# Kernel tuning notes

Hardware: AMD Instinct MI355X
Metric: run time of the kernel (lower is better)

## Reference

```python
import jax, jax.numpy as jnp
import numpy as np

H = 16        # query heads
HK = 8        # kv heads
D = 128       # head dim
HID = 2048    # hidden size
FF = 6144     # mlp intermediate
THETA = 1e6   # rope base (qwen3)
EPS = 1e-6
T = 2048      # total tokens


def rmsnorm(x, w):
    return x * jax.lax.rsqrt(jnp.mean(x * x, axis=-1, keepdims=True) + EPS) * w


def rope(pos, x):
    # x: [T, h, D], rotate-half RoPE
    half = D // 2
    inv = 1.0 / (THETA ** (jnp.arange(half, dtype=jnp.float32) / half))
    freqs = pos.astype(jnp.float32)[:, None] * inv          # [T, half]
    cos = jnp.cos(freqs)[:, None, :]
    sin = jnp.sin(freqs)[:, None, :]
    x1, x2 = x[..., :half], x[..., half:]
    return jnp.concatenate([x1 * cos - x2 * sin, x2 * cos + x1 * sin], axis=-1)


def setup_inputs() -> dict:
    key = jax.random.key(0)
    ks = jax.random.split(key, 12)
    s = 0.02
    return {
        "positions": jnp.arange(T, dtype=jnp.int32),
        "hidden_states": jax.random.normal(ks[0], (T, HID), dtype=jnp.float32),
        "wq": jax.random.normal(ks[1], (H * D, HID), dtype=jnp.float32) * s,
        "wk": jax.random.normal(ks[2], (HK * D, HID), dtype=jnp.float32) * s,
        "wv": jax.random.normal(ks[3], (HK * D, HID), dtype=jnp.float32) * s,
        "wo": jax.random.normal(ks[4], (HID, H * D), dtype=jnp.float32) * s,
        "q_norm_w": jnp.ones((D,), dtype=jnp.float32),
        "k_norm_w": jnp.ones((D,), dtype=jnp.float32),
        "ln1_w": jnp.ones((HID,), dtype=jnp.float32),
        "ln2_w": jnp.ones((HID,), dtype=jnp.float32),
        "w_gate": jax.random.normal(ks[5], (FF, HID), dtype=jnp.float32) * s,
        "w_up": jax.random.normal(ks[6], (FF, HID), dtype=jnp.float32) * s,
        "w_down": jax.random.normal(ks[7], (HID, FF), dtype=jnp.float32) * s,
    }


def reference(positions, hidden_states, wq, wk, wv, wo, q_norm_w, k_norm_w,
              ln1_w, ln2_w, w_gate, w_up, w_down):
    t = hidden_states.shape[0]
    residual = hidden_states
    h = rmsnorm(hidden_states, ln1_w)
    q = (h @ wq.T).reshape(t, H, D)
    k = (h @ wk.T).reshape(t, HK, D)
    v = (h @ wv.T).reshape(t, HK, D)
    q = rmsnorm(q, q_norm_w)
    k = rmsnorm(k, k_norm_w)
    q = rope(positions, q)
    k = rope(positions, k)
    # GQA: expand kv heads to query heads
    g = H // HK
    kr = jnp.repeat(k, g, axis=1)  # [t, H, D]
    vr = jnp.repeat(v, g, axis=1)
    scores = jnp.einsum('thd,shd->hts', q, kr) * (D ** -0.5)
    causal = positions[:, None] >= positions[None, :]
    scores = jnp.where(causal[None], scores, jnp.finfo(scores.dtype).min)
    p = jax.nn.softmax(scores, axis=-1)
    o = jnp.einsum('hts,shd->thd', p, vr).reshape(t, H * D)
    h = residual + o @ wo.T
    residual = h
    h = rmsnorm(h, ln2_w)
    h = (jax.nn.silu(h @ w_gate.T) * (h @ w_up.T)) @ w_down.T
    return residual + h
```

## Files before the change

### kernel.cpp

```cpp
#include <hip/hip_runtime.h>
#include <hip/hip_bf16.h>
#include <stdint.h>

namespace {

constexpr int kT   = 2048;
constexpr int kHid = 2048;
constexpr int kH   = 16;
constexpr int kHK  = 8;
constexpr int kD   = 128;
constexpr int kFF  = 6144;

using bf16x8 = __attribute__((ext_vector_type(8))) short;
using f32x4  = __attribute__((ext_vector_type(4))) float;

__device__ __forceinline__ float bf2f(unsigned short u) {
    return __uint_as_float(((unsigned)u) << 16);
}
__device__ __forceinline__ unsigned short f2bf(float f) {
    unsigned u = __float_as_uint(f);
    return (unsigned short)((u + 0x7fffu + ((u >> 16) & 1u)) >> 16);
}
__device__ __forceinline__ void gload_lds16(const void* g, void* l) {
    __builtin_amdgcn_global_load_lds(
        (__attribute__((address_space(1))) void*)g,
        (__attribute__((address_space(3))) void*)l, 16, 0, 0);
}
__device__ __forceinline__ f32x4 mf(bf16x8 a, bf16x8 b, f32x4 c) {
    return __builtin_amdgcn_mfma_f32_16x16x32_bf16(a, b, c, 0, 0, 0);
}

__global__ __launch_bounds__(256)
void cvt_f32_bf16(const float* __restrict__ src, unsigned short* __restrict__ dst, int n4) {
    int i = blockIdx.x * 256 + threadIdx.x;
    if (i < n4) {
        float4 v = ((const float4*)src)[i];
        ushort4 o;
        o.x = f2bf(v.x); o.y = f2bf(v.y); o.z = f2bf(v.z); o.w = f2bf(v.w);
        ((ushort4*)dst)[i] = o;
    }
}

__global__ __launch_bounds__(256)
void reduce2(const float* __restrict__ p0, const float* __restrict__ p1,
             const float* __restrict__ res, float* __restrict__ out, int n4) {
    int i = blockIdx.x * 256 + threadIdx.x;
    if (i < n4) {
        float4 a = ((const float4*)p0)[i];
        float4 b = ((const float4*)p1)[i];
        float4 r = ((const float4*)res)[i];
        float4 o;
        o.x = a.x + b.x + r.x;
        o.y = a.y + b.y + r.y;
        o.z = a.z + b.z + r.z;
        o.w = a.w + b.w + r.w;
        ((float4*)out)[i] = o;
    }
}

__global__ __launch_bounds__(256)
void rmsnorm_k(const float* __restrict__ x, const float* __restrict__ w,
               unsigned short* __restrict__ out) {
    const int row = blockIdx.x;
    const int tid = threadIdx.x;
    const float4* xr = (const float4*)(x + (size_t)row * kHid);
    float4 v0 = xr[tid];
    float4 v1 = xr[tid + 256];
    float ss = v0.x*v0.x + v0.y*v0.y + v0.z*v0.z + v0.w*v0.w
             + v1.x*v1.x + v1.y*v1.y + v1.z*v1.z + v1.w*v1.w;
#pragma unroll
    for (int m = 1; m < 64; m <<= 1) ss += __shfl_xor(ss, m);
    __shared__ float red[4];
    if ((tid & 63) == 0) red[tid >> 6] = ss;
    __syncthreads();
    float tot = red[0] + red[1] + red[2] + red[3];
    float rs = rsqrtf(tot * (1.0f / kHid) + 1e-6f);
    const float4* wv = (const float4*)w;
    float4 w0 = wv[tid], w1 = wv[tid + 256];
    ushort4 o0, o1;
    o0.x = f2bf(v0.x * rs * w0.x); o0.y = f2bf(v0.y * rs * w0.y);
    o0.z = f2bf(v0.z * rs * w0.z); o0.w = f2bf(v0.w * rs * w0.w);
    o1.x = f2bf(v1.x * rs * w1.x); o1.y = f2bf(v1.y * rs * w1.y);
    o1.z = f2bf(v1.z * rs * w1.z); o1.w = f2bf(v1.w * rs * w1.w);
    ushort4* orow = (ushort4*)(out + (size_t)row * kHid);
    orow[tid] = o0;
    orow[tid + 256] = o1;
}

template <int EPI>
__global__ __launch_bounds__(512, 2)
void gemm128(const unsigned short* __restrict__ A,
             const unsigned short* __restrict__ B,
             void* __restrict__ C,
             int M, int N, int K, int KS,
             float* __restrict__ p0, float* __restrict__ p1) {
    __shared__ unsigned short smem[2][3][128 * 64];

    const int tid  = threadIdx.x;
    const int lane = tid & 63;
    const int l15  = lane & 15;
    const int g4   = lane >> 4;
    const int wid  = tid >> 6;
    const int wr   = wid >> 2;
    const int wc   = wid & 3;
    const int bm   = blockIdx.y * 128;
    const int bn   = blockIdx.x * 256;
    const int kb   = (EPI == 4) ? blockIdx.z * KS : 0;
    const int NT   = ((EPI == 4) ? KS : K) >> 6;
    const int NI   = NT >> 1;

    f32x4 acc[4][4] = {};

    auto stage = [&](int b, int reg, int t) {
        const unsigned short* Base = (reg == 0) ? A : B;
        const int br = (reg == 0) ? bm : bn + (reg - 1) * 128;
#pragma unroll
        for (int i = 0; i < 2; ++i) {
            int ch   = tid + i * 512;
            int row  = ch >> 3;
            int slot = (ch & 7) ^ (row & 7);
            gload_lds16(Base + (size_t)(br + row) * K + kb + t * 64 + slot * 8,
                        (char*)&smem[b][reg][0] + ch * 16);
        }
    };
    auto rdA = [&](int b, int m, int ks) {
        int row = wr * 64 + m * 16 + l15;
        return *(const bf16x8*)((const char*)&smem[b][0][0]
               + row * 128 + (((ks * 4 + g4) ^ (row & 7)) * 16));
    };
    auto rdB = [&](int b, int n, int ks) {
        int row = wc * 64 + n * 16 + l15;
        return *(const bf16x8*)((const char*)&smem[b][1 + (row >> 7)][0]
               + (row & 127) * 128 + (((ks * 4 + g4) ^ (row & 7)) * 16));
    };

    stage(0, 1, 0); stage(0, 2, 0); stage(0, 0, 0);
    stage(1, 1, 1); stage(1, 2, 1);
    asm volatile("s_waitcnt vmcnt(4)" ::: "memory");
    __builtin_amdgcn_s_barrier();

    for (int i = 0; i < NI; ++i) {
        const int e  = 2 * i;
        const int o  = e + 1;
        const bool pf = (e + 2 < NT);
        bf16x8 af[4][2], bfr[4][2];

#pragma unroll
        for (int m = 0; m < 4; ++m) { af[m][0] = rdA(0, m, 0); af[m][1] = rdA(0, m, 1); }
#pragma unroll
        for (int n = 0; n < 4; ++n) { bfr[n][0] = rdB(0, n, 0); bfr[n][1] = rdB(0, n, 1); }
        stage(1, 0, o);
        __builtin_amdgcn_s_barrier();
        asm volatile("s_waitcnt lgkmcnt(0)" ::: "memory");
        __builtin_amdgcn_sched_barrier(0);
        __builtin_amdgcn_s_setprio(1);
#pragma unroll
        for (int m = 0; m < 4; ++m) {
            acc[m][0] = mf(af[m][0], bfr[0][0], acc[m][0]);
            acc[m][0] = mf(af[m][1], bfr[0][1], acc[m][0]);
        }
        __builtin_amdgcn_s_setprio(0);
        __builtin_amdgcn_s_barrier();

        if (pf) stage(0, 1, e + 2);
        __builtin_amdgcn_s_barrier();
        __builtin_amdgcn_s_setprio(1);
#pragma unroll
        for (int m = 0; m < 4; ++m) {
            acc[m][1] = mf(af[m][0], bfr[1][0], acc[m][1]);
            acc[m][1] = mf(af[m][1], bfr[1][1], acc[m][1]);
        }
        __builtin_amdgcn_s_setprio(0);
        __builtin_amdgcn_s_barrier();

        if (pf) stage(0, 2, e + 2);
        __builtin_amdgcn_s_barrier();
        __builtin_amdgcn_s_setprio(1);
#pragma unroll
        for (int m = 0; m < 4; ++m) {
            acc[m][2] = mf(af[m][0], bfr[2][0], acc[m][2]);
            acc[m][2] = mf(af[m][1], bfr[2][1], acc[m][2]);
        }
        __builtin_amdgcn_s_setprio(0);
        __builtin_amdgcn_s_barrier();

        __builtin_amdgcn_s_setprio(1);
#pragma unroll
        for (int m = 0; m < 4; ++m) {
            acc[m][3] = mf(af[m][0], bfr[3][0], acc[m][3]);
            acc[m][3] = mf(af[m][1], bfr[3][1], acc[m][3]);
        }
        __builtin_amdgcn_s_setprio(0);
        if (pf) asm volatile("s_waitcnt vmcnt(4)" ::: "memory");
        else    asm volatile("s_waitcnt vmcnt(0)" ::: "memory");
        __builtin_amdgcn_s_barrier();

#pragma unroll
        for (int m = 0; m < 4; ++m) { af[m][0] = rdA(1, m, 0); af[m][1] = rdA(1, m, 1); }
#pragma unroll
        for (int n = 0; n < 4; ++n) { bfr[n][0] = rdB(1, n, 0); bfr[n][1] = rdB(1, n, 1); }
        if (pf) stage(0, 0, e + 2);
        __builtin_amdgcn_s_barrier();
        asm volatile("s_waitcnt lgkmcnt(0)" ::: "memory");
        __builtin_amdgcn_sched_barrier(0);
        __builtin_amdgcn_s_setprio(1);
#pragma unroll
        for (int m = 0; m < 4; ++m) {
            acc[m][0] = mf(af[m][0], bfr[0][0], acc[m][0]);
            acc[m][0] = mf(af[m][1], bfr[0][1], acc[m][0]);
        }
        __builtin_amdgcn_s_setprio(0);
        __builtin_amdgcn_s_barrier();

        if (pf) stage(1, 1, o + 2);
        __builtin_amdgcn_s_barrier();
        __builtin_amdgcn_s_setprio(1);
#pragma unroll
        for (int m = 0; m < 4; ++m) {
            acc[m][1] = mf(af[m][0], bfr[1][0], acc[m][1]);
            acc[m][1] = mf(af[m][1], bfr[1][1], acc[m][1]);
        }
        __builtin_amdgcn_s_setprio(0);
        __builtin_amdgcn_s_barrier();

        if (pf) stage(1, 2, o + 2);
        __builtin_amdgcn_s_barrier();
        __builtin_amdgcn_s_setprio(1);
#pragma unroll
        for (int m = 0; m < 4; ++m) {
            acc[m][2] = mf(af[m][0], bfr[2][0], acc[m][2]);
            acc[m][2] = mf(af[m][1], bfr[2][1], acc[m][2]);
        }
        __builtin_amdgcn_s_setprio(0);
        __builtin_amdgcn_s_barrier();

        __builtin_amdgcn_s_setprio(1);
#pragma unroll
        for (int m = 0; m < 4; ++m) {
            acc[m][3] = mf(af[m][0], bfr[3][0], acc[m][3]);
            acc[m][3] = mf(af[m][1], bfr[3][1], acc[m][3]);
        }
        __builtin_amdgcn_s_setprio(0);
        if (pf) asm volatile("s_waitcnt vmcnt(4)" ::: "memory");
        __builtin_amdgcn_s_barrier();
    }

    float* P = nullptr;
    if (EPI == 4) P = (blockIdx.z == 0) ? p0 : p1;
#pragma unroll
    for (int m = 0; m < 4; ++m) {
#pragma unroll
        for (int n = 0; n < 4; ++n) {
            int row = bm + wr * 64 + m * 16 + g4 * 4;
            int col = bn + wc * 64 + n * 16 + l15;
#pragma unroll
            for (int r = 0; r < 4; ++r) {
                size_t idx = (size_t)(row + r) * N + col;
                float v = acc[m][n][r];
                if (EPI == 0) ((float*)C)[idx] = v;
                else          P[idx] = v;
            }
        }
    }
}

__global__ __launch_bounds__(512, 2)
void gemm_gu(const unsigned short* __restrict__ A,
             const unsigned short* __restrict__ WGp,
             const unsigned short* __restrict__ WUp,
             unsigned short* __restrict__ OUT) {
    __shared__ unsigned short smem[2][4][128 * 64];

    const int tid  = threadIdx.x;
    const int lane = tid & 63;
    const int l15  = lane & 15;
    const int g4   = lane >> 4;
    const int wid  = tid >> 6;
    const int wr   = wid >> 1;
    const int wc   = wid & 1;
    const int bm   = blockIdx.y * 256;
    const int bn2  = blockIdx.x * 128;
    const int K    = kHid;
    const int NT   = K >> 6;
    const int NI   = NT >> 1;

    f32x4 accg[4][4] = {};
    f32x4 accu[4][4] = {};

    auto stage = [&](int b, int reg, int t) {
        const unsigned short* Base = (reg == 2) ? WGp : (reg == 3) ? WUp : A;
        const int br = (reg < 2) ? (bm + reg * 128) : bn2;
#pragma unroll
        for (int i = 0; i < 2; ++i) {
            int ch   = tid + i * 512;
            int row  = ch >> 3;
            int slot = (ch & 7) ^ (row & 7);
            gload_lds16(Base + (size_t)(br + row) * K + t * 64 + slot * 8,
                        (char*)&smem[b][reg][0] + ch * 16);
        }
    };
    auto rdA = [&](int b, int m, int ks) {
        int rt  = wr * 64 + m * 16 + l15;
        int row = rt & 127;
        return *(const bf16x8*)((const char*)&smem[b][rt >> 7][0]
               + row * 128 + (((ks * 4 + g4) ^ (row & 7)) * 16));
    };
    auto rdB = [&](int b, int reg, int n, int ks) {
        int row = wc * 64 + n * 16 + l15;
        return *(const bf16x8*)((const char*)&smem[b][reg][0]
               + row * 128 + (((ks * 4 + g4) ^ (row & 7)) * 16));
    };

    stage(0, 2, 0); stage(0, 3, 0); stage(0, 0, 0); stage(0, 1, 0);
    stage(1, 2, 1); stage(1, 0, 1); stage(1, 1, 1);
    asm volatile("s_waitcnt vmcnt(6)" ::: "memory");
    __builtin_amdgcn_s_barrier();

    for (int i = 0; i < NI; ++i) {
        const int e  = 2 * i;
        const int o  = e + 1;
        const bool pf = (e + 2 < NT);
        bf16x8 af[4][2], bg[4][2], bu[4][2];

#pragma unroll
        for (int m = 0; m < 4; ++m) { af[m][0] = rdA(0, m, 0); af[m][1] = rdA(0, m, 1); }
#pragma unroll
        for (int n = 0; n < 4; ++n) { bg[n][0] = rdB(0, 2, n, 0); bg[n][1] = rdB(0, 2, n, 1); }
        stage(1, 3, o);
        __builtin_amdgcn_s_barrier();
        asm volatile("s_waitcnt lgkmcnt(0)" ::: "memory");
        __builtin_amdgcn_sched_barrier(0);
        __builtin_amdgcn_s_setprio(1);
#pragma unroll
        for (int m = 0; m < 4; ++m)
#pragma unroll
            for (int n = 0; n < 2; ++n) {
                accg[m][n] = mf(af[m][0], bg[n][0], accg[m][n]);
                accg[m][n] = mf(af[m][1], bg[n][1], accg[m][n]);
            }
        __builtin_amdgcn_s_setprio(0);
        __builtin_amdgcn_s_barrier();

        if (pf) stage(0, 2, e + 2);
        __builtin_amdgcn_s_barrier();
        __builtin_amdgcn_s_setprio(1);
#pragma unroll
        for (int m = 0; m < 4; ++m)
#pragma unroll
            for (int n = 2; n < 4; ++n) {
                accg[m][n] = mf(af[m][0], bg[n][0], accg[m][n]);
                accg[m][n] = mf(af[m][1], bg[n][1], accg[m][n]);
            }
        __builtin_amdgcn_s_setprio(0);
        __builtin_amdgcn_s_barrier();

#pragma unroll
        for (int n = 0; n < 4; ++n) { bu[n][0] = rdB(0, 3, n, 0); bu[n][1] = rdB(0, 3, n, 1); }
        if (pf) stage(0, 0, e + 2);
        __builtin_amdgcn_s_barrier();
        asm volatile("s_waitcnt lgkmcnt(0)" ::: "memory");
        __builtin_amdgcn_sched_barrier(0);
        __builtin_amdgcn_s_setprio(1);
#pragma unroll
        for (int m = 0; m < 4; ++m)
#pragma unroll
            for (int n = 0; n < 2; ++n) {
                accu[m][n] = mf(af[m][0], bu[n][0], accu[m][n]);
                accu[m][n] = mf(af[m][1], bu[n][1], accu[m][n]);
            }
        __builtin_amdgcn_s_setprio(0);
        __builtin_amdgcn_s_barrier();

        if (pf) stage(0, 1, e + 2);
        __builtin_amdgcn_s_barrier();
        __builtin_amdgcn_s_setprio(1);
#pragma unroll
        for (int m = 0; m < 4; ++m)
#pragma unroll
            for (int n = 2; n < 4; ++n) {
                accu[m][n] = mf(af[m][0], bu[n][0], accu[m][n]);
                accu[m][n] = mf(af[m][1], bu[n][1], accu[m][n]);
            }
        __builtin_amdgcn_s_setprio(0);
        if (pf) asm volatile("s_waitcnt vmcnt(6)" ::: "memory");
        else    asm volatile("s_waitcnt vmcnt(0)" ::: "memory");
        __builtin_amdgcn_s_barrier();

#pragma unroll
        for (int m = 0; m < 4; ++m) { af[m][0] = rdA(1, m, 0); af[m][1] = rdA(1, m, 1); }
#pragma unroll
        for (int n = 0; n < 4; ++n) { bg[n][0] = rdB(1, 2, n, 0); bg[n][1] = rdB(1, 2, n, 1); }
        if (pf) stage(0, 3, e + 2);
        __builtin_amdgcn_s_barrier();
        asm volatile("s_waitcnt lgkmcnt(0)" ::: "memory");
        __builtin_amdgcn_sched_barrier(0);
        __builtin_amdgcn_s_setprio(1);
#pragma unroll
        for (int m = 0; m < 4; ++m)
#pragma unroll
            for (int n = 0; n < 2; ++n) {
                accg[m][n] = mf(af[m][0], bg[n][0], accg[m][n]);
                accg[m][n] = mf(af[m][1], bg[n][1], accg[m][n]);
            }
        __builtin_amdgcn_s_setprio(0);
        __builtin_amdgcn_s_barrier();

        if (pf) stage(1, 2, o + 2);
        __builtin_amdgcn_s_barrier();
        __builtin_amdgcn_s_setprio(1);
#pragma unroll
        for (int m = 0; m < 4; ++m)
#pragma unroll
            for (int n = 2; n < 4; ++n) {
                accg[m][n] = mf(af[m][0], bg[n][0], accg[m][n]);
                accg[m][n] = mf(af[m][1], bg[n][1], accg[m][n]);
            }
        __builtin_amdgcn_s_setprio(0);
        __builtin_amdgcn_s_barrier();

#pragma unroll
        for (int n = 0; n < 4; ++n) { bu[n][0] = rdB(1, 3, n, 0); bu[n][1] = rdB(1, 3, n, 1); }
        if (pf) stage(1, 0, o + 2);
        __builtin_amdgcn_s_barrier();
        asm volatile("s_waitcnt lgkmcnt(0)" ::: "memory");
        __builtin_amdgcn_sched_barrier(0);
        __builtin_amdgcn_s_setprio(1);
#pragma unroll
        for (int m = 0; m < 4; ++m)
#pragma unroll
            for (int n = 0; n < 2; ++n) {
                accu[m][n] = mf(af[m][0], bu[n][0], accu[m][n]);
                accu[m][n] = mf(af[m][1], bu[n][1], accu[m][n]);
            }
        __builtin_amdgcn_s_setprio(0);
        __builtin_amdgcn_s_barrier();

        if (pf) stage(1, 1, o + 2);
        __builtin_amdgcn_s_barrier();
        __builtin_amdgcn_s_setprio(1);
#pragma unroll
        for (int m = 0; m < 4; ++m)
#pragma unroll
            for (int n = 2; n < 4; ++n) {
                accu[m][n] = mf(af[m][0], bu[n][0], accu[m][n]);
                accu[m][n] = mf(af[m][1], bu[n][1], accu[m][n]);
            }
        __builtin_amdgcn_s_setprio(0);
        if (pf) asm volatile("s_waitcnt vmcnt(6)" ::: "memory");
        __builtin_amdgcn_s_barrier();
    }

#pragma unroll
    for (int m = 0; m < 4; ++m) {
#pragma unroll
        for (int n = 0; n < 4; ++n) {
            int row = bm + wr * 64 + m * 16 + g4 * 4;
            int col = bn2 + wc * 64 + n * 16 + l15;
#pragma unroll
            for (int r = 0; r < 4; ++r) {
                float g = accg[m][n][r];
                float u = accu[m][n][r];
                OUT[(size_t)(row + r) * kFF + col] = f2bf(g / (1.0f + __expf(-g)) * u);
            }
        }
    }
}

__global__ __launch_bounds__(256)
void qknorm_rope(const float* __restrict__ qkv, const int* __restrict__ positions,
                 const float* __restrict__ qnw, const float* __restrict__ knw,
                 unsigned short* __restrict__ Qo, unsigned short* __restrict__ Ko) {
    const int t    = blockIdx.x;
    const int j    = blockIdx.y * 4 + (threadIdx.x >> 6);
    const int lane = threadIdx.x & 63;
    const float* src = qkv + (size_t)t * 4096 + j * 128;
    float x1 = src[lane];
    float x2 = src[lane + 64];
    float ss = x1 * x1 + x2 * x2;
#pragma unroll
    for (int m = 1; m < 64; m <<= 1) ss += __shfl_xor(ss, m);
    float rs = rsqrtf(ss * (1.0f / 128.0f) + 1e-6f);
    const float* w = (j < 16) ? qnw : knw;
    float n1 = x1 * rs * w[lane];
    float n2 = x2 * rs * w[lane + 64];
    float inv = powf(1.0e6f, -(float)lane * (1.0f / 64.0f));
    float fr = (float)positions[t] * inv;
    float sn, cs;
    sincosf(fr, &sn, &cs);
    float o1 = n1 * cs - n2 * sn;
    float o2 = n2 * cs + n1 * sn;
    if (j < 16) {
        unsigned short* d = Qo + (size_t)t * (kH * kD) + j * kD;
        d[lane] = f2bf(o1);
        d[lane + 64] = f2bf(o2);
    } else {
        unsigned short* d = Ko + (size_t)t * (kHK * kD) + (j - 16) * kD;
        d[lane] = f2bf(o1);
        d[lane + 64] = f2bf(o2);
    }
}

__global__ __launch_bounds__(256)
void vtrans(const float* __restrict__ qkv, unsigned short* __restrict__ Vt) {
    __shared__ float tile[32][33];
    const int t0 = blockIdx.x * 32;
    const int d0 = blockIdx.y * 32;
    const int tc = threadIdx.x & 31;
    const int tr = threadIdx.x >> 5;
#pragma unroll
    for (int i = 0; i < 4; ++i) {
        int trow = tr + i * 8;
        tile[trow][tc] = qkv[(size_t)(t0 + trow) * 4096 + 3072 + d0 + tc];
    }
    __syncthreads();
#pragma unroll
    for (int i = 0; i < 4; ++i) {
        int drow = tr + i * 8;
        Vt[(size_t)(d0 + drow) * kT + t0 + tc] = f2bf(tile[tc][drow]);
    }
}

__global__ __launch_bounds__(512, 4)
void attn_fwd5(const unsigned short* __restrict__ Q,
               const unsigned short* __restrict__ Kc,
               const unsigned short* __restrict__ Vt,
               unsigned short* __restrict__ O) {
    __shared__ unsigned short Kb[2][64 * 128];
    __shared__ unsigned short Vb[2][128 * 64];
    __shared__ float MergeML[4][2][64];

    const int tid  = threadIdx.x;
    const int lane = tid & 63;
    const int l15  = lane & 15;
    const int g4   = lane >> 4;
    const int wid  = tid >> 6;
    const int s    = wid & 1;
    const int grp  = wid >> 1;
    const int hs   = grp >> 1;
    const int qsub = grp & 1;
    const int hkk  = blockIdx.x;
    const int h    = hkk * 2 + hs;
    const int nby  = gridDim.y;
    const int by   = blockIdx.y;
    const int byl  = (by & 1) ? (nby - 1 - (by >> 1)) : (by >> 1);
    const int q0   = byl * 32 + qsub * 16;
    const int nch  = byl / 2 + 1;
    const int c0   = (nch + 1) >> 1;
    const int myn  = s ? (nch - c0) : c0;
    const int qi   = q0 + l15;
    const int vt   = grp * 64 + lane;

    const int addrA = ((g4 & 1) * 32 + l15) * 4;
    const int addrB = addrA + 64;
    const int addrQ = g4 * 80;
    const bool hb   = (g4 >> 1) != 0;

    bf16x8 qf[4];
#pragma unroll
    for (int ks = 0; ks < 4; ++ks)
        qf[ks] = *(const bf16x8*)(Q + (size_t)(q0 + l15) * (kH * kD) + h * kD + ks * 32 + g4 * 8);

    f32x4 oacc[8] = {};
    float mrun = -3e38f, lrun = 0.f;
    const float scale = 0.08838834764831845f;

    auto stage = [&](int kv0) {
#pragma unroll
        for (int i = 0; i < 4; ++i) {
            int ch  = vt + i * 256;
            int row = ch >> 4;
            int c16 = ch & 15;
            gload_lds16(Kc + (size_t)(kv0 + row) * (kHK * kD) + hkk * kD
                            + ((c16 ^ (row & 7)) * 8),
                        (char*)Kb[s] + ch * 16);
        }
#pragma unroll
        for (int i = 0; i < 4; ++i) {
            int ch  = vt + i * 256;
            int row = ch >> 3;
            int c8  = ch & 7;
            gload_lds16(Vt + (size_t)(hkk * kD + row) * kT + kv0
                            + ((c8 ^ (row & 7)) * 8),
                        (char*)Vb[s] + ch * 16);
        }
    };

    for (int c = 0; c < c0; ++c) {
        const bool act = c < myn;
        const int kv0 = (s ? (c0 + c) : c) * 64;
        if (act) stage(kv0);
        asm volatile("s_waitcnt vmcnt(0)" ::: "memory");
        __builtin_amdgcn_s_barrier();
        __builtin_amdgcn_sched_barrier(0);

        if (act) {
            f32x4 sa[4] = {};
            __builtin_amdgcn_s_setprio(1);
#pragma unroll
            for (int hh = 0; hh < 4; ++hh) {
                const int row = hh * 16 + l15;
#pragma unroll
                for (int ks = 0; ks < 4; ++ks) {
                    bf16x8 kf = *(const bf16x8*)((const char*)Kb[s]
                                  + row * 256 + (((ks * 4 + g4) ^ (row & 7)) * 16));
                    sa[hh] = mf(kf, qf[ks], sa[hh]);
                }
            }
            __builtin_amdgcn_s_setprio(0);

            float sv[4][4];
#pragma unroll
            for (int hh = 0; hh < 4; ++hh)
#pragma unroll
                for (int r = 0; r < 4; ++r)
                    sv[hh][r] = sa[hh][r] * scale;
            if (kv0 + 63 > q0) {
#pragma unroll
                for (int hh = 0; hh < 4; ++hh)
#pragma unroll
                    for (int r = 0; r < 4; ++r) {
                        int ki = kv0 + hh * 16 + g4 * 4 + r;
                        if (ki > qi) sv[hh][r] = -3e38f;
                    }
            }

            float m16;
            {
                float a = fmaxf(fmaxf(sv[0][0], sv[0][1]), fmaxf(sv[0][2], sv[0][3]));
                float b2 = fmaxf(fmaxf(sv[1][0], sv[1][1]), fmaxf(sv[1][2], sv[1][3]));
                float c2 = fmaxf(fmaxf(sv[2][0], sv[2][1]), fmaxf(sv[2][2], sv[2][3]));
                float d2 = fmaxf(fmaxf(sv[3][0], sv[3][1]), fmaxf(sv[3][2], sv[3][3]));
                m16 = fmaxf(fmaxf(a, b2), fmaxf(c2, d2));
            }
            m16 = fmaxf(m16, __shfl_xor(m16, 16));
            m16 = fmaxf(m16, __shfl_xor(m16, 32));

            if (__any(m16 > mrun)) {
                float mnew = fmaxf(mrun, m16);
                float corr = __expf(mrun - mnew);
                mrun = mnew;
                lrun *= corr;
                float cr[4];
#pragma unroll
                for (int r = 0; r < 4; ++r)
                    cr[r] = __int_as_float(__builtin_amdgcn_ds_bpermute(
                                addrQ + 4 * r, __float_as_int(corr)));
#pragma unroll
                for (int c2 = 0; c2 < 8; ++c2)
#pragma unroll
                    for (int r = 0; r < 4; ++r)
                        oacc[c2][r] *= cr[r];
            }

            float p[4][4];
            float ps = 0.f;
#pragma unroll
            for (int hh = 0; hh < 4; ++hh)
#pragma unroll
                for (int r = 0; r < 4; ++r) {
                    float pe = __expf(sv[hh][r] - mrun);
                    p[hh][r] = pe;
                    ps += pe;
                }
            ps += __shfl_xor(ps, 16);
            ps += __shfl_xor(ps, 32);
            lrun += ps;

            unsigned pk[4][2];
#pragma unroll
            for (int hh = 0; hh < 4; ++hh) {
                asm("v_cvt_pk_bf16_f32 %0, %1, %2"
                    : "=v"(pk[hh][0]) : "v"(p[hh][0]), "v"(p[hh][1]));
                asm("v_cvt_pk_bf16_f32 %0, %1, %2"
                    : "=v"(pk[hh][1]) : "v"(p[hh][2]), "v"(p[hh][3]));
            }
            int ex[4][2][2];
#pragma unroll
            for (int hh = 0; hh < 4; ++hh)
#pragma unroll
                for (int ii = 0; ii < 2; ++ii) {
                    ex[hh][ii][0] = __builtin_amdgcn_ds_bpermute(addrA, (int)pk[hh][ii]);
                    ex[hh][ii][1] = __builtin_amdgcn_ds_bpermute(addrB, (int)pk[hh][ii]);
                }
            union { int w[4]; bf16x8 v; } pu0, pu1;
#pragma unroll
            for (int jw = 0; jw < 4; ++jw) {
                pu0.w[jw] = hb ? ex[1][jw & 1][jw >> 1] : ex[0][jw & 1][jw >> 1];
                pu1.w[jw] = hb ? ex[3][jw & 1][jw >> 1] : ex[2][jw & 1][jw >> 1];
            }
            bf16x8 pa0 = pu0.v;
            bf16x8 pa1 = pu1.v;

            __builtin_amdgcn_s_setprio(1);
#pragma unroll
            for (int c2 = 0; c2 < 8; ++c2) {
                const int d = c2 * 16 + l15;
                bf16x8 vf0 = *(const bf16x8*)((const char*)Vb[s]
                              + d * 128 + ((g4 ^ (d & 7)) * 16));
                oacc[c2] = mf(pa0, vf0, oacc[c2]);
                bf16x8 vf1 = *(const bf16x8*)((const char*)Vb[s]
                              + d * 128 + ((((4 + g4) ^ (d & 7))) * 16));
                oacc[c2] = mf(pa1, vf1, oacc[c2]);
            }
            __builtin_amdgcn_s_setprio(0);
        }
        __builtin_amdgcn_s_barrier();
    }

    float* KbF = (float*)&Kb[0][0];
    if (s == 1) {
        MergeML[grp][0][lane] = mrun;
        MergeML[grp][1][lane] = lrun;
#pragma unroll
        for (int c2 = 0; c2 < 8; ++c2)
#pragma unroll
            for (int r = 0; r < 4; ++r)
                KbF[grp * 2048 + (c2 * 4 + r) * 64 + lane] = oacc[c2][r];
    }
    asm volatile("s_waitcnt lgkmcnt(0)" ::: "memory");
    __builtin_amdgcn_s_barrier();

    if (s == 0) {
        float m1 = MergeML[grp][0][lane];
        float l1 = MergeML[grp][1][lane];
        float mg = fmaxf(mrun, m1);
        float a0 = __expf(mrun - mg);
        float a1 = __expf(m1 - mg);
        float L  = lrun * a0 + l1 * a1;
        float ar0[4], ar1[4], Lr[4];
#pragma unroll
        for (int r = 0; r < 4; ++r) {
            ar0[r] = __int_as_float(__builtin_amdgcn_ds_bpermute(
                         addrQ + 4 * r, __float_as_int(a0)));
            ar1[r] = __int_as_float(__builtin_amdgcn_ds_bpermute(
                         addrQ + 4 * r, __float_as_int(a1)));
            Lr[r]  = __int_as_float(__builtin_amdgcn_ds_bpermute(
                         addrQ + 4 * r, __float_as_int(L)));
        }
#pragma unroll
        for (int c2 = 0; c2 < 8; ++c2)
#pragma unroll
            for (int r = 0; r < 4; ++r) {
                float oex = KbF[grp * 2048 + (c2 * 4 + r) * 64 + lane];
                float v = (oacc[c2][r] * ar0[r] + oex * ar1[r]) / Lr[r];
                O[(size_t)(q0 + g4 * 4 + r) * (kH * kD) + h * kD + c2 * 16 + l15] = f2bf(v);
            }
    }
}

}

extern "C" void kernel_launch(void* const* d_in, const int* in_sizes, int n_in,
                              void* d_out, int out_size, void* d_ws, size_t ws_size,
                              hipStream_t stream) {
    (void)in_sizes; (void)n_in; (void)out_size; (void)ws_size;

    const int*   positions = (const int*)  d_in[0];
    const float* hidden    = (const float*)d_in[1];
    const float* wq  = (const float*)d_in[2];
    const float* wk  = (const float*)d_in[3];
    const float* wv  = (const float*)d_in[4];
    const float* wo  = (const float*)d_in[5];
    const float* qnw = (const float*)d_in[6];
    const float* knw = (const float*)d_in[7];
    const float* ln1 = (const float*)d_in[8];
    const float* ln2 = (const float*)d_in[9];
    const float* wg  = (const float*)d_in[10];
    const float* wu  = (const float*)d_in[11];
    const float* wd  = (const float*)d_in[12];

    char* ws = (char*)d_ws;
    unsigned short* WQKV = (unsigned short*)(ws + 0);
    unsigned short* WO   = (unsigned short*)(ws + 16777216);
    unsigned short* WG   = (unsigned short*)(ws + 25165824);
    unsigned short* WU   = (unsigned short*)(ws + 50331648);
    unsigned short* WD   = (unsigned short*)(ws + 75497472);
    unsigned short* XN1  = (unsigned short*)(ws + 100663296);
    unsigned short* OATT = (unsigned short*)(ws + 109051904);
    float*          H1   = (float*)(ws + 117440512);
    unsigned short* XN2  = (unsigned short*)(ws + 134217728);
    float*          QKVF = (float*)(ws + 142606336);
    unsigned short* QB   = (unsigned short*)(ws + 176160768);
    unsigned short* KB   = (unsigned short*)(ws + 184549376);
    unsigned short* VT   = (unsigned short*)(ws + 188743680);
    unsigned short* ACT  = (unsigned short*)(ws + 167772160);

    float* OP0 = (float*)(ws + 142606336);
    float* OP1 = (float*)(ws + 159383552);
    float* DP0 = (float*)(ws + 0);
    float* DP1 = (float*)(ws + 16777216);

    auto cvt = [&](const float* s, unsigned short* dst, size_t n) {
        int n4 = (int)(n / 4);
        cvt_f32_bf16<<<dim3((n4 + 255) / 256), dim3(256), 0, stream>>>(s, dst, n4);
    };

    cvt(wq, WQKV,                 (size_t)kH  * kD * kHid);
    cvt(wk, WQKV + 2048 * kHid,   (size_t)kHK * kD * kHid);
    cvt(wv, WQKV + 3072 * kHid,   (size_t)kHK * kD * kHid);
    cvt(wo, WO,                   (size_t)kHid * kH * kD);
    cvt(wg, WG,                   (size_t)kFF * kHid);
    cvt(wu, WU,                   (size_t)kFF * kHid);
    cvt(wd, WD,                   (size_t)kHid * kFF);

    rmsnorm_k<<<dim3(kT), dim3(256), 0, stream>>>(hidden, ln1, XN1);

    gemm128<0><<<dim3(4096 / 256, kT / 128), dim3(512), 0, stream>>>(
        XN1, WQKV, QKVF, kT, 4096, kHid, kHid, nullptr, nullptr);

    qknorm_rope<<<dim3(kT, 6), dim3(256), 0, stream>>>(QKVF, positions, qnw, knw, QB, KB);
    vtrans<<<dim3(kT / 32, 1024 / 32), dim3(256), 0, stream>>>(QKVF, VT);

    attn_fwd5<<<dim3(kHK, kT / 32), dim3(512), 0, stream>>>(QB, KB, VT, OATT);

    gemm128<4><<<dim3(kHid / 256, kT / 128, 2), dim3(512), 0, stream>>>(
        OATT, WO, nullptr, kT, kHid, kHid, 1024, OP0, OP1);
    reduce2<<<dim3(kT * kHid / 4 / 256), dim3(256), 0, stream>>>(
        OP0, OP1, hidden, H1, kT * kHid / 4);

    rmsnorm_k<<<dim3(kT), dim3(256), 0, stream>>>(H1, ln2, XN2);

    gemm_gu<<<dim3(kFF / 128, kT / 256), dim3(512), 0, stream>>>(XN2, WG, WU, ACT);

    gemm128<4><<<dim3(kHid / 256, kT / 128, 2), dim3(512), 0, stream>>>(
        ACT, WD, nullptr, kT, kHid, kFF, 3072, DP0, DP1);
    reduce2<<<dim3(kT * kHid / 4 / 256), dim3(256), 0, stream>>>(
        DP0, DP1, H1, (float*)d_out, kT * kHid / 4);
}
```

Measured before the change: 396.6 us.

## Use 256x256 split-K-4 GEMMs, fuse reduction into RMSNorm, retile gate/up GEMM

```diff
diff --git a/kernel.cpp b/kernel.cpp
--- a/kernel.cpp
+++ b/kernel.cpp
@@ -42,18 +42,21 @@
 }
 
 __global__ __launch_bounds__(256)
-void reduce2(const float* __restrict__ p0, const float* __restrict__ p1,
+void reduce4(const float* __restrict__ p0, const float* __restrict__ p1,
+             const float* __restrict__ p2, const float* __restrict__ p3,
              const float* __restrict__ res, float* __restrict__ out, int n4) {
     int i = blockIdx.x * 256 + threadIdx.x;
     if (i < n4) {
         float4 a = ((const float4*)p0)[i];
         float4 b = ((const float4*)p1)[i];
+        float4 c = ((const float4*)p2)[i];
+        float4 d = ((const float4*)p3)[i];
         float4 r = ((const float4*)res)[i];
         float4 o;
-        o.x = a.x + b.x + r.x;
-        o.y = a.y + b.y + r.y;
-        o.z = a.z + b.z + r.z;
-        o.w = a.w + b.w + r.w;
+        o.x = a.x + b.x + c.x + d.x + r.x;
+        o.y = a.y + b.y + c.y + d.y + r.y;
+        o.z = a.z + b.z + c.z + d.z + r.z;
+        o.w = a.w + b.w + c.w + d.w + r.w;
         ((float4*)out)[i] = o;
     }
 }
@@ -87,6 +90,265 @@
     orow[tid + 256] = o1;
 }
 
+__global__ __launch_bounds__(256)
+void rmsnorm_red4(const float* __restrict__ p0, const float* __restrict__ p1,
+                  const float* __restrict__ p2, const float* __restrict__ p3,
+                  const float* __restrict__ res, const float* __restrict__ w,
+                  float* __restrict__ H, unsigned short* __restrict__ out) {
+    const int row = blockIdx.x;
+    const int tid = threadIdx.x;
+    const size_t base = (size_t)row * kHid;
+    float4 v0, v1;
+    {
+        const float4* a = (const float4*)(p0 + base);
+        const float4* b = (const float4*)(p1 + base);
+        const float4* c = (const float4*)(p2 + base);
+        const float4* d = (const float4*)(p3 + base);
+        const float4* r = (const float4*)(res + base);
+        float4 a0 = a[tid], b0 = b[tid], c0 = c[tid], d0 = d[tid], r0 = r[tid];
+        v0.x = a0.x + b0.x + c0.x + d0.x + r0.x;
+        v0.y = a0.y + b0.y + c0.y + d0.y + r0.y;
+        v0.z = a0.z + b0.z + c0.z + d0.z + r0.z;
+        v0.w = a0.w + b0.w + c0.w + d0.w + r0.w;
+        float4 a1 = a[tid + 256], b1 = b[tid + 256], c1 = c[tid + 256],
+               d1 = d[tid + 256], r1 = r[tid + 256];
+        v1.x = a1.x + b1.x + c1.x + d1.x + r1.x;
+        v1.y = a1.y + b1.y + c1.y + d1.y + r1.y;
+        v1.z = a1.z + b1.z + c1.z + d1.z + r1.z;
+        v1.w = a1.w + b1.w + c1.w + d1.w + r1.w;
+    }
+    ((float4*)(H + base))[tid] = v0;
+    ((float4*)(H + base))[tid + 256] = v1;
+    float ss = v0.x*v0.x + v0.y*v0.y + v0.z*v0.z + v0.w*v0.w
+             + v1.x*v1.x + v1.y*v1.y + v1.z*v1.z + v1.w*v1.w;
+#pragma unroll
+    for (int m = 1; m < 64; m <<= 1) ss += __shfl_xor(ss, m);
+    __shared__ float red[4];
+    if ((tid & 63) == 0) red[tid >> 6] = ss;
+    __syncthreads();
+    float tot = red[0] + red[1] + red[2] + red[3];
+    float rs = rsqrtf(tot * (1.0f / kHid) + 1e-6f);
+    const float4* wv = (const float4*)w;
+    float4 w0 = wv[tid], w1 = wv[tid + 256];
+    ushort4 o0, o1;
+    o0.x = f2bf(v0.x * rs * w0.x); o0.y = f2bf(v0.y * rs * w0.y);
+    o0.z = f2bf(v0.z * rs * w0.z); o0.w = f2bf(v0.w * rs * w0.w);
+    o1.x = f2bf(v1.x * rs * w1.x); o1.y = f2bf(v1.y * rs * w1.y);
+    o1.z = f2bf(v1.z * rs * w1.z); o1.w = f2bf(v1.w * rs * w1.w);
+    ushort4* orow = (ushort4*)(out + base);
+    orow[tid] = o0;
+    orow[tid + 256] = o1;
+}
+
+template <int EPI>
+__global__ __launch_bounds__(512, 2)
+void gemm256(const unsigned short* __restrict__ A,
+             const unsigned short* __restrict__ B,
+             void* __restrict__ C,
+             int M, int N, int K, int KS,
+             float* __restrict__ p0, float* __restrict__ p1,
+             float* __restrict__ p2, float* __restrict__ p3) {
+    __shared__ unsigned short smem[2][4][128 * 64];
+
+    const int tid  = threadIdx.x;
+    const int lane = tid & 63;
+    const int l15  = lane & 15;
+    const int g4   = lane >> 4;
+    const int wid  = tid >> 6;
+    const int wr   = wid >> 2;
+    const int wc   = wid & 3;
+    const int bm   = blockIdx.y * 256;
+    const int bn   = blockIdx.x * 256;
+    const int kb   = (EPI == 4) ? blockIdx.z * KS : 0;
+    const int NT   = ((EPI == 4) ? KS : K) >> 6;
+    const int NI   = NT >> 1;
+
+    f32x4 acc[8][4] = {};
+
+    auto stage = [&](int b, int reg, int t) {
+        const unsigned short* Base = (reg < 2) ? A : B;
+        const int br = ((reg < 2) ? bm : bn) + (reg & 1) * 128;
+#pragma unroll
+        for (int i = 0; i < 2; ++i) {
+            int ch   = tid + i * 512;
+            int row  = ch >> 3;
+            int slot = (ch & 7) ^ (row & 7);
+            gload_lds16(Base + (size_t)(br + row) * K + kb + t * 64 + slot * 8,
+                        (char*)&smem[b][reg][0] + ch * 16);
+        }
+    };
+    auto rdA = [&](int b, int m, int ks) {
+        int row = m * 16 + l15;
+        return *(const bf16x8*)((const char*)&smem[b][wr][0]
+               + row * 128 + (((ks * 4 + g4) ^ (row & 7)) * 16));
+    };
+    auto rdB = [&](int b, int n, int ks) {
+        int row = wc * 64 + n * 16 + l15;
+        return *(const bf16x8*)((const char*)&smem[b][2 + (row >> 7)][0]
+               + (row & 127) * 128 + (((ks * 4 + g4) ^ (row & 7)) * 16));
+    };
+
+    stage(0, 2, 0); stage(0, 3, 0); stage(0, 0, 0); stage(0, 1, 0);
+    stage(1, 2, 1); stage(1, 3, 1); stage(1, 0, 1);
+    asm volatile("s_waitcnt vmcnt(6)" ::: "memory");
+    __builtin_amdgcn_s_barrier();
+
+    for (int i = 0; i < NI; ++i) {
+        const int e  = 2 * i;
+        const int o  = e + 1;
+        const bool pf = (e + 2 < NT);
+        bf16x8 af[4][2], bfr[4][2];
+
+#pragma unroll
+        for (int m = 0; m < 4; ++m) { af[m][0] = rdA(0, m, 0); af[m][1] = rdA(0, m, 1); }
+#pragma unroll
+        for (int n = 0; n < 4; ++n) { bfr[n][0] = rdB(0, n, 0); bfr[n][1] = rdB(0, n, 1); }
+        stage(1, 1, o);
+        __builtin_amdgcn_s_barrier();
+        asm volatile("s_waitcnt lgkmcnt(0)" ::: "memory");
+        __builtin_amdgcn_sched_barrier(0);
+        __builtin_amdgcn_s_setprio(1);
+#pragma unroll
+        for (int m = 0; m < 4; ++m)
+#pragma unroll
+            for (int n = 0; n < 2; ++n) {
+                acc[m][n] = mf(af[m][0], bfr[n][0], acc[m][n]);
+                acc[m][n] = mf(af[m][1], bfr[n][1], acc[m][n]);
+            }
+        __builtin_amdgcn_s_setprio(0);
+        __builtin_amdgcn_s_barrier();
+
+        if (pf) stage(0, 2, e + 2);
+        __builtin_amdgcn_s_barrier();
+        __builtin_amdgcn_s_setprio(1);
+#pragma unroll
+        for (int m = 0; m < 4; ++m)
+#pragma unroll
+            for (int n = 2; n < 4; ++n) {
+                acc[m][n] = mf(af[m][0], bfr[n][0], acc[m][n]);
+                acc[m][n] = mf(af[m][1], bfr[n][1], acc[m][n]);
+            }
+        __builtin_amdgcn_s_setprio(0);
+        __builtin_amdgcn_s_barrier();
+
+#pragma unroll
+        for (int m = 0; m < 4; ++m) { af[m][0] = rdA(0, 4 + m, 0); af[m][1] = rdA(0, 4 + m, 1); }
+        if (pf) stage(0, 3, e + 2);
+        __builtin_amdgcn_s_barrier();
+        asm volatile("s_waitcnt lgkmcnt(0)" ::: "memory");
+        __builtin_amdgcn_sched_barrier(0);
+        __builtin_amdgcn_s_setprio(1);
+#pragma unroll
+        for (int m = 0; m < 4; ++m)
+#pragma unroll
+            for (int n = 0; n < 2; ++n) {
+                acc[4 + m][n] = mf(af[m][0], bfr[n][0], acc[4 + m][n]);
+                acc[4 + m][n] = mf(af[m][1], bfr[n][1], acc[4 + m][n]);
+            }
+        __builtin_amdgcn_s_setprio(0);
+        __builtin_amdgcn_s_barrier();
+
+        if (pf) stage(0, 0, e + 2);
+        __builtin_amdgcn_s_barrier();
+        __builtin_amdgcn_s_setprio(1);
+#pragma unroll
+        for (int m = 0; m < 4; ++m)
+#pragma unroll
+            for (int n = 2; n < 4; ++n) {
+                acc[4 + m][n] = mf(af[m][0], bfr[n][0], acc[4 + m][n]);
+                acc[4 + m][n] = mf(af[m][1], bfr[n][1], acc[4 + m][n]);
+            }
+        __builtin_amdgcn_s_setprio(0);
+        if (pf) asm volatile("s_waitcnt vmcnt(6)" ::: "memory");
+        else    asm volatile("s_waitcnt vmcnt(0)" ::: "memory");
+        __builtin_amdgcn_s_barrier();
+
+#pragma unroll
+        for (int m = 0; m < 4; ++m) { af[m][0] = rdA(1, m, 0); af[m][1] = rdA(1, m, 1); }
+#pragma unroll
+        for (int n = 0; n < 4; ++n) { bfr[n][0] = rdB(1, n, 0); bfr[n][1] = rdB(1, n, 1); }
+        if (pf) stage(0, 1, e + 2);
+        __builtin_amdgcn_s_barrier();
+        asm volatile("s_waitcnt lgkmcnt(0)" ::: "memory");
+        __builtin_amdgcn_sched_barrier(0);
+        __builtin_amdgcn_s_setprio(1);
+#pragma unroll
+        for (int m = 0; m < 4; ++m)
+#pragma unroll
+            for (int n = 0; n < 2; ++n) {
+                acc[m][n] = mf(af[m][0], bfr[n][0], acc[m][n]);
+                acc[m][n] = mf(af[m][1], bfr[n][1], acc[m][n]);
+            }
+        __builtin_amdgcn_s_setprio(0);
+        __builtin_amdgcn_s_barrier();
+
+        if (pf) stage(1, 2, o + 2);
+        __builtin_amdgcn_s_barrier();
+        __builtin_amdgcn_s_setprio(1);
+#pragma unroll
+        for (int m = 0; m < 4; ++m)
+#pragma unroll
+            for (int n = 2; n < 4; ++n) {
+                acc[m][n] = mf(af[m][0], bfr[n][0], acc[m][n]);
+                acc[m][n] = mf(af[m][1], bfr[n][1], acc[m][n]);
+            }
+        __builtin_amdgcn_s_setprio(0);
+        __builtin_amdgcn_s_barrier();
+
+#pragma unroll
+        for (int m = 0; m < 4; ++m) { af[m][0] = rdA(1, 4 + m, 0); af[m][1] = rdA(1, 4 + m, 1); }
+        if (pf) stage(1, 3, o + 2);
+        __builtin_amdgcn_s_barrier();
+        asm volatile("s_waitcnt lgkmcnt(0)" ::: "memory");
+        __builtin_amdgcn_sched_barrier(0);
+        __builtin_amdgcn_s_setprio(1);
+#pragma unroll
+        for (int m = 0; m < 4; ++m)
+#pragma unroll
+            for (int n = 0; n < 2; ++n) {
+                acc[4 + m][n] = mf(af[m][0], bfr[n][0], acc[4 + m][n]);
+                acc[4 + m][n] = mf(af[m][1], bfr[n][1], acc[4 + m][n]);
+            }
+        __builtin_amdgcn_s_setprio(0);
+        __builtin_amdgcn_s_barrier();
+
+        if (pf) stage(1, 0, o + 2);
+        __builtin_amdgcn_s_barrier();
+        __builtin_amdgcn_s_setprio(1);
+#pragma unroll
+        for (int m = 0; m < 4; ++m)
+#pragma unroll
+            for (int n = 2; n < 4; ++n) {
+                acc[4 + m][n] = mf(af[m][0], bfr[n][0], acc[4 + m][n]);
+                acc[4 + m][n] = mf(af[m][1], bfr[n][1], acc[4 + m][n]);
+            }
+        __builtin_amdgcn_s_setprio(0);
+        if (pf) asm volatile("s_waitcnt vmcnt(6)" ::: "memory");
+        __builtin_amdgcn_s_barrier();
+    }
+
+    float* P = nullptr;
+    if (EPI == 4) {
+        const int z = blockIdx.z;
+        P = (z == 0) ? p0 : (z == 1) ? p1 : (z == 2) ? p2 : p3;
+    }
+#pragma unroll
+    for (int m = 0; m < 8; ++m) {
+#pragma unroll
+        for (int n = 0; n < 4; ++n) {
+            int row = bm + wr * 128 + m * 16 + g4 * 4;
+            int col = bn + wc * 64 + n * 16 + l15;
+#pragma unroll
+            for (int r = 0; r < 4; ++r) {
+                size_t idx = (size_t)(row + r) * N + col;
+                float v = acc[m][n][r];
+                if (EPI == 0) ((float*)C)[idx] = v;
+                else          P[idx] = v;
+            }
+        }
+    }
+}
+
 template <int EPI>
 __global__ __launch_bounds__(512, 2)
 void gemm128(const unsigned short* __restrict__ A,
@@ -269,7 +531,7 @@
              const unsigned short* __restrict__ WGp,
              const unsigned short* __restrict__ WUp,
              unsigned short* __restrict__ OUT) {
-    __shared__ unsigned short smem[2][4][128 * 64];
+    __shared__ unsigned short smem[2][28672];
 
     const int tid  = threadIdx.x;
     const int lane = tid & 63;
@@ -279,54 +541,74 @@
     const int wr   = wid >> 1;
     const int wc   = wid & 1;
     const int bm   = blockIdx.y * 256;
-    const int bn2  = blockIdx.x * 128;
+    const int bn   = blockIdx.x * 96;
     const int K    = kHid;
     const int NT   = K >> 6;
     const int NI   = NT >> 1;
 
-    f32x4 accg[4][4] = {};
-    f32x4 accu[4][4] = {};
-
-    auto stage = [&](int b, int reg, int t) {
-        const unsigned short* Base = (reg == 2) ? WGp : (reg == 3) ? WUp : A;
-        const int br = (reg < 2) ? (bm + reg * 128) : bn2;
+    f32x4 accg[4][3] = {};
+    f32x4 accu[4][3] = {};
+
+    constexpr int OFF_A0 = 0;
+    constexpr int OFF_A1 = 16384;
+    constexpr int OFF_GU = 32768;
+
+    auto stage_a = [&](int b, int half, int t) {
 #pragma unroll
         for (int i = 0; i < 2; ++i) {
             int ch   = tid + i * 512;
             int row  = ch >> 3;
             int slot = (ch & 7) ^ (row & 7);
-            gload_lds16(Base + (size_t)(br + row) * K + t * 64 + slot * 8,
-                        (char*)&smem[b][reg][0] + ch * 16);
+            gload_lds16(A + (size_t)(bm + half * 128 + row) * K + t * 64 + slot * 8,
+                        (char*)&smem[b][0] + (half ? OFF_A1 : OFF_A0) + ch * 16);
+        }
+    };
+    auto stage_gu = [&](int b, int t) {
+#pragma unroll
+        for (int i = 0; i < 3; ++i) {
+            int ch   = tid + i * 512;
+            int row  = ch >> 3;
+            int slot = (ch & 7) ^ (row & 7);
+            const unsigned short* Base = (row >= 96) ? WUp : WGp;
+            int srow = bn + (row >= 96 ? row - 96 : row);
+            gload_lds16(Base + (size_t)srow * K + t * 64 + slot * 8,
+                        (char*)&smem[b][0] + OFF_GU + ch * 16);
         }
     };
     auto rdA = [&](int b, int m, int ks) {
         int rt  = wr * 64 + m * 16 + l15;
         int row = rt & 127;
-        return *(const bf16x8*)((const char*)&smem[b][rt >> 7][0]
+        return *(const bf16x8*)((const char*)&smem[b][0]
+               + (rt >> 7 ? OFF_A1 : OFF_A0)
                + row * 128 + (((ks * 4 + g4) ^ (row & 7)) * 16));
     };
-    auto rdB = [&](int b, int reg, int n, int ks) {
-        int row = wc * 64 + n * 16 + l15;
-        return *(const bf16x8*)((const char*)&smem[b][reg][0]
+    auto rdG = [&](int b, int n, int ks) {
+        int row = wc * 48 + n * 16 + l15;
+        return *(const bf16x8*)((const char*)&smem[b][0] + OFF_GU
                + row * 128 + (((ks * 4 + g4) ^ (row & 7)) * 16));
     };
-
-    stage(0, 2, 0); stage(0, 3, 0); stage(0, 0, 0); stage(0, 1, 0);
-    stage(1, 2, 1); stage(1, 0, 1); stage(1, 1, 1);
-    asm volatile("s_waitcnt vmcnt(6)" ::: "memory");
+    auto rdU = [&](int b, int n, int ks) {
+        int row = 96 + wc * 48 + n * 16 + l15;
+        return *(const bf16x8*)((const char*)&smem[b][0] + OFF_GU
+               + row * 128 + (((ks * 4 + g4) ^ (row & 7)) * 16));
+    };
+
+    stage_a(0, 0, 0); stage_a(0, 1, 0); stage_gu(0, 0);
+    stage_a(1, 0, 1); stage_a(1, 1, 1);
+    asm volatile("s_waitcnt vmcnt(4)" ::: "memory");
     __builtin_amdgcn_s_barrier();
 
     for (int i = 0; i < NI; ++i) {
         const int e  = 2 * i;
         const int o  = e + 1;
         const bool pf = (e + 2 < NT);
-        bf16x8 af[4][2], bg[4][2], bu[4][2];
+        bf16x8 af[4][2], bg[3][2], bu[3][2];
 
 #pragma unroll
         for (int m = 0; m < 4; ++m) { af[m][0] = rdA(0, m, 0); af[m][1] = rdA(0, m, 1); }
 #pragma unroll
-        for (int n = 0; n < 4; ++n) { bg[n][0] = rdB(0, 2, n, 0); bg[n][1] = rdB(0, 2, n, 1); }
-        stage(1, 3, o);
+        for (int n = 0; n < 3; ++n) { bg[n][0] = rdG(0, n, 0); bg[n][1] = rdG(0, n, 1); }
+        stage_gu(1, o);
         __builtin_amdgcn_s_barrier();
         asm volatile("s_waitcnt lgkmcnt(0)" ::: "memory");
         __builtin_amdgcn_sched_barrier(0);
@@ -334,29 +616,25 @@
 #pragma unroll
         for (int m = 0; m < 4; ++m)
 #pragma unroll
-            for (int n = 0; n < 2; ++n) {
+            for (int n = 0; n < 3; ++n)
                 accg[m][n] = mf(af[m][0], bg[n][0], accg[m][n]);
+        __builtin_amdgcn_s_setprio(0);
+        __builtin_amdgcn_s_barrier();
+
+        if (pf) stage_a(0, 0, e + 2);
+        __builtin_amdgcn_s_barrier();
+        __builtin_amdgcn_s_setprio(1);
+#pragma unroll
+        for (int m = 0; m < 4; ++m)
+#pragma unroll
+            for (int n = 0; n < 3; ++n)
                 accg[m][n] = mf(af[m][1], bg[n][1], accg[m][n]);
-            }
-        __builtin_amdgcn_s_setprio(0);
-        __builtin_amdgcn_s_barrier();
-
-        if (pf) stage(0, 2, e + 2);
-        __builtin_amdgcn_s_barrier();
-        __builtin_amdgcn_s_setprio(1);
-#pragma unroll
-        for (int m = 0; m < 4; ++m)
-#pragma unroll
-            for (int n = 2; n < 4; ++n) {
-                accg[m][n] = mf(af[m][0], bg[n][0], accg[m][n]);
-                accg[m][n] = mf(af[m][1], bg[n][1], accg[m][n]);
-            }
-        __builtin_amdgcn_s_setprio(0);
-        __builtin_amdgcn_s_barrier();
-
-#pragma unroll
-        for (int n = 0; n < 4; ++n) { bu[n][0] = rdB(0, 3, n, 0); bu[n][1] = rdB(0, 3, n, 1); }
-        if (pf) stage(0, 0, e + 2);
+        __builtin_amdgcn_s_setprio(0);
+        __builtin_amdgcn_s_barrier();
+
+#pragma unroll
+        for (int n = 0; n < 3; ++n) { bu[n][0] = rdU(0, n, 0); bu[n][1] = rdU(0, n, 1); }
+        if (pf) stage_a(0, 1, e + 2);
         __builtin_amdgcn_s_barrier();
         asm volatile("s_waitcnt lgkmcnt(0)" ::: "memory");
         __builtin_amdgcn_sched_barrier(0);
@@ -364,33 +642,28 @@
 #pragma unroll
         for (int m = 0; m < 4; ++m)
 #pragma unroll
-            for (int n = 0; n < 2; ++n) {
+            for (int n = 0; n < 3; ++n)
                 accu[m][n] = mf(af[m][0], bu[n][0], accu[m][n]);
+        __builtin_amdgcn_s_setprio(0);
+        __builtin_amdgcn_s_barrier();
+
+        if (pf) stage_gu(0, e + 2);
+        __builtin_amdgcn_s_barrier();
+        __builtin_amdgcn_s_setprio(1);
+#pragma unroll
+        for (int m = 0; m < 4; ++m)
+#pragma unroll
+            for (int n = 0; n < 3; ++n)
                 accu[m][n] = mf(af[m][1], bu[n][1], accu[m][n]);
-            }
-        __builtin_amdgcn_s_setprio(0);
-        __builtin_amdgcn_s_barrier();
-
-        if (pf) stage(0, 1, e + 2);
-        __builtin_amdgcn_s_barrier();
-        __builtin_amdgcn_s_setprio(1);
-#pragma unroll
-        for (int m = 0; m < 4; ++m)
-#pragma unroll
-            for (int n = 2; n < 4; ++n) {
-                accu[m][n] = mf(af[m][0], bu[n][0], accu[m][n]);
-                accu[m][n] = mf(af[m][1], bu[n][1], accu[m][n]);
-            }
-        __builtin_amdgcn_s_setprio(0);
-        if (pf) asm volatile("s_waitcnt vmcnt(6)" ::: "memory");
+        __builtin_amdgcn_s_setprio(0);
+        if (pf) asm volatile("s_waitcnt vmcnt(7)" ::: "memory");
         else    asm volatile("s_waitcnt vmcnt(0)" ::: "memory");
         __builtin_amdgcn_s_barrier();
 
 #pragma unroll
         for (int m = 0; m < 4; ++m) { af[m][0] = rdA(1, m, 0); af[m][1] = rdA(1, m, 1); }
 #pragma unroll
-        for (int n = 0; n < 4; ++n) { bg[n][0] = rdB(1, 2, n, 0); bg[n][1] = rdB(1, 2, n, 1); }
-        if (pf) stage(0, 3, e + 2);
+        for (int n = 0; n < 3; ++n) { bg[n][0] = rdG(1, n, 0); bg[n][1] = rdG(1, n, 1); }
         __builtin_amdgcn_s_barrier();
         asm volatile("s_waitcnt lgkmcnt(0)" ::: "memory");
         __builtin_amdgcn_sched_barrier(0);
@@ -398,29 +671,25 @@
 #pragma unroll
         for (int m = 0; m < 4; ++m)
 #pragma unroll
-            for (int n = 0; n < 2; ++n) {
+            for (int n = 0; n < 3; ++n)
                 accg[m][n] = mf(af[m][0], bg[n][0], accg[m][n]);
+        __builtin_amdgcn_s_setprio(0);
+        __builtin_amdgcn_s_barrier();
+
+        if (pf) stage_a(1, 0, o + 2);
+        __builtin_amdgcn_s_barrier();
+        __builtin_amdgcn_s_setprio(1);
+#pragma unroll
+        for (int m = 0; m < 4; ++m)
+#pragma unroll
+            for (int n = 0; n < 3; ++n)
                 accg[m][n] = mf(af[m][1], bg[n][1], accg[m][n]);
-            }
-        __builtin_amdgcn_s_setprio(0);
-        __builtin_amdgcn_s_barrier();
-
-        if (pf) stage(1, 2, o + 2);
-        __builtin_amdgcn_s_barrier();
-        __builtin_amdgcn_s_setprio(1);
-#pragma unroll
-        for (int m = 0; m < 4; ++m)
-#pragma unroll
-            for (int n = 2; n < 4; ++n) {
-                accg[m][n] = mf(af[m][0], bg[n][0], accg[m][n]);
-                accg[m][n] = mf(af[m][1], bg[n][1], accg[m][n]);
-            }
-        __builtin_amdgcn_s_setprio(0);
-        __builtin_amdgcn_s_barrier();
-
-#pragma unroll
-        for (int n = 0; n < 4; ++n) { bu[n][0] = rdB(1, 3, n, 0); bu[n][1] = rdB(1, 3, n, 1); }
-        if (pf) stage(1, 0, o + 2);
+        __builtin_amdgcn_s_setprio(0);
+        __builtin_amdgcn_s_barrier();
+
+#pragma unroll
+        for (int n = 0; n < 3; ++n) { bu[n][0] = rdU(1, n, 0); bu[n][1] = rdU(1, n, 1); }
+        if (pf) stage_a(1, 1, o + 2);
         __builtin_amdgcn_s_barrier();
         asm volatile("s_waitcnt lgkmcnt(0)" ::: "memory");
         __builtin_amdgcn_sched_barrier(0);
@@ -428,34 +697,28 @@
 #pragma unroll
         for (int m = 0; m < 4; ++m)
 #pragma unroll
-            for (int n = 0; n < 2; ++n) {
+            for (int n = 0; n < 3; ++n)
                 accu[m][n] = mf(af[m][0], bu[n][0], accu[m][n]);
+        __builtin_amdgcn_s_setprio(0);
+        __builtin_amdgcn_s_barrier();
+
+        __builtin_amdgcn_s_setprio(1);
+#pragma unroll
+        for (int m = 0; m < 4; ++m)
+#pragma unroll
+            for (int n = 0; n < 3; ++n)
                 accu[m][n] = mf(af[m][1], bu[n][1], accu[m][n]);
-            }
-        __builtin_amdgcn_s_setprio(0);
-        __builtin_amdgcn_s_barrier();
-
-        if (pf) stage(1, 1, o + 2);
-        __builtin_amdgcn_s_barrier();
-        __builtin_amdgcn_s_setprio(1);
-#pragma unroll
-        for (int m = 0; m < 4; ++m)
-#pragma unroll
-            for (int n = 2; n < 4; ++n) {
-                accu[m][n] = mf(af[m][0], bu[n][0], accu[m][n]);
-                accu[m][n] = mf(af[m][1], bu[n][1], accu[m][n]);
-            }
-        __builtin_amdgcn_s_setprio(0);
-        if (pf) asm volatile("s_waitcnt vmcnt(6)" ::: "memory");
+        __builtin_amdgcn_s_setprio(0);
+        if (pf) asm volatile("s_waitcnt vmcnt(4)" ::: "memory");
         __builtin_amdgcn_s_barrier();
     }
 
 #pragma unroll
     for (int m = 0; m < 4; ++m) {
 #pragma unroll
-        for (int n = 0; n < 4; ++n) {
+        for (int n = 0; n < 3; ++n) {
             int row = bm + wr * 64 + m * 16 + g4 * 4;
-            int col = bn2 + wc * 64 + n * 16 + l15;
+            int col = bn + wc * 48 + n * 16 + l15;
 #pragma unroll
             for (int r = 0; r < 4; ++r) {
                 float g = accg[m][n][r];
@@ -787,8 +1050,12 @@
 
     float* OP0 = (float*)(ws + 142606336);
     float* OP1 = (float*)(ws + 159383552);
+    float* OP2 = (float*)(ws + 176160768);
+    float* OP3 = (float*)(ws + 0);
     float* DP0 = (float*)(ws + 0);
     float* DP1 = (float*)(ws + 16777216);
+    float* DP2 = (float*)(ws + 33554432);
+    float* DP3 = (float*)(ws + 142606336);
 
     auto cvt = [&](const float* s, unsigned short* dst, size_t n) {
         int n4 = (int)(n / 4);
@@ -813,17 +1080,15 @@
 
     attn_fwd5<<<dim3(kHK, kT / 32), dim3(512), 0, stream>>>(QB, KB, VT, OATT);
 
-    gemm128<4><<<dim3(kHid / 256, kT / 128, 2), dim3(512), 0, stream>>>(
-        OATT, WO, nullptr, kT, kHid, kHid, 1024, OP0, OP1);
-    reduce2<<<dim3(kT * kHid / 4 / 256), dim3(256), 0, stream>>>(
-        OP0, OP1, hidden, H1, kT * kHid / 4);
-
-    rmsnorm_k<<<dim3(kT), dim3(256), 0, stream>>>(H1, ln2, XN2);
-
-    gemm_gu<<<dim3(kFF / 128, kT / 256), dim3(512), 0, stream>>>(XN2, WG, WU, ACT);
-
-    gemm128<4><<<dim3(kHid / 256, kT / 128, 2), dim3(512), 0, stream>>>(
-        ACT, WD, nullptr, kT, kHid, kFF, 3072, DP0, DP1);
-    reduce2<<<dim3(kT * kHid / 4 / 256), dim3(256), 0, stream>>>(
-        DP0, DP1, H1, (float*)d_out, kT * kHid / 4);
-}
+    gemm256<4><<<dim3(kHid / 256, kT / 256, 4), dim3(512), 0, stream>>>(
+        OATT, WO, nullptr, kT, kHid, kHid, 512, OP0, OP1, OP2, OP3);
+    rmsnorm_red4<<<dim3(kT), dim3(256), 0, stream>>>(
+        OP0, OP1, OP2, OP3, hidden, ln2, H1, XN2);
+
+    gemm_gu<<<dim3(kFF / 96, kT / 256), dim3(512), 0, stream>>>(XN2, WG, WU, ACT);
+
+    gemm256<4><<<dim3(kHid / 256, kT / 256, 4), dim3(512), 0, stream>>>(
+        ACT, WD, nullptr, kT, kHid, kFF, 1536, DP0, DP1, DP2, DP3);
+    reduce4<<<dim3(kT * kHid / 4 / 256), dim3(256), 0, stream>>>(
+        DP0, DP1, DP2, DP3, H1, (float*)d_out, kT * kHid / 4);
+}
```

New measurement: 386.3 us (median of 2 runs). 1.03x faster.
